# Kernel tuning notes

Measured on AMD Instinct MI355X. Metric: run time of the kernel, lower is better.

## Reference

```python
import jax, jax.numpy as jnp
import numpy as np

B, P, T, F, H, C = 256, 5, 256, 128, 512, 60
R_ON = 0.05    # open ratio of the phased-LSTM time gate
ALPHA = 0.001  # leak during the closed phase


def setup_inputs() -> dict:
    key = jax.random.key(0)
    ks = jax.random.split(key, 8)
    D = P * F  # flattened per-step input to the cell
    s = 1.0 / np.sqrt(H)
    inputs = jax.random.normal(ks[0], (B, P, T, F), dtype=jnp.float32)
    Wx = jax.random.uniform(ks[1], (D, 4 * H), minval=-s, maxval=s, dtype=jnp.float32)
    Wh = jax.random.uniform(ks[2], (H, 4 * H), minval=-s, maxval=s, dtype=jnp.float32)
    b = jax.random.uniform(ks[3], (4 * H,), minval=-s, maxval=s, dtype=jnp.float32)
    # time-gate params: periods spread log-uniformly up to seq length, random phase
    tau = jnp.exp(jax.random.uniform(ks[4], (H,), minval=0.0, maxval=np.log(T), dtype=jnp.float32)) + 1.0
    shift = jax.random.uniform(ks[5], (H,), minval=0.0, maxval=float(T), dtype=jnp.float32)
    fc_w = jax.random.uniform(ks[6], (H, C), minval=-s, maxval=s, dtype=jnp.float32)
    fc_b = jax.random.uniform(ks[7], (C,), minval=-s, maxval=s, dtype=jnp.float32)
    return {"inputs": inputs, "Wx": Wx, "Wh": Wh, "b": b,
            "tau": tau, "shift": shift, "fc_w": fc_w, "fc_b": fc_b}


def _time_gate(t, tau, shift):
    # phase in [0,1); triangular opening of width r_on, alpha leak otherwise
    phi = jnp.mod(t - shift, tau) / tau  # (H,)
    up = 2.0 * phi / R_ON
    down = 2.0 - up
    return jnp.where(phi < 0.5 * R_ON, up,
                     jnp.where(phi < R_ON, down, ALPHA * phi))


def reference(inputs, Wx, Wh, b, tau, shift, fc_w, fc_b):
    # inputs: (B, P, T, F) -> time-major flattened (T, B, P*F)
    x_seq = jnp.transpose(inputs, (2, 0, 1, 3)).reshape(T, B, P * F)
    times = jnp.arange(T, dtype=jnp.float32)

    h0 = jnp.zeros((B, H), dtype=inputs.dtype)
    c0 = jnp.zeros((B, H), dtype=inputs.dtype)

    def step(carry, xt):
        h, c = carry
        x, t = xt
        gates = x @ Wx + h @ Wh + b          # (B, 4H)
        i, f, g, o = jnp.split(gates, 4, axis=-1)
        i = jax.nn.sigmoid(i)
        f = jax.nn.sigmoid(f)
        g = jnp.tanh(g)
        o = jax.nn.sigmoid(o)
        c_tilde = f * c + i * g              # LSTM cell proposal
        h_tilde = o * jnp.tanh(c_tilde)
        k = _time_gate(t, tau, shift)        # (H,) phased time gate
        c_new = k * c_tilde + (1.0 - k) * c
        h_new = k * h_tilde + (1.0 - k) * h
        return (h_new, c_new), None

    (hT, _), _ = jax.lax.scan(step, (h0, c0), (x_seq, times))
    logits = hT @ fc_w + fc_b                # (B, C)
    return jax.nn.log_softmax(logits, axis=-1)
```

## Files before the change

### kernel.cpp

```cpp
#include <hip/hip_runtime.h>
#include <math.h>

#define T_STEPS 256
#define BATCH   256
#define HID     512
#define DIN     640
#define NCOL    2048
#define NCLASS  60
#define KSTEPS  36
#define KX      20
#define KH      16

typedef float f32x4 __attribute__((ext_vector_type(4)));
typedef short s16x8 __attribute__((ext_vector_type(8)));

#define WF_OFF   4096
#define HB0_OFF  4722688
#define HB1_OFF  4984832
#define HPL_OFF  5246976
#define XF_OFF   5771264
#define WS_NEED  89657344ULL

__device__ __forceinline__ unsigned short f2bf(float x) {
    union { float f; unsigned u; } v; v.f = x;
    unsigned r = v.u + 0x7fffu + ((v.u >> 16) & 1u);
    return (unsigned short)(r >> 16);
}

__device__ __forceinline__ s16x8 pack8(float4 a, float4 b) {
    s16x8 r;
    r[0] = (short)f2bf(a.x); r[1] = (short)f2bf(a.y);
    r[2] = (short)f2bf(a.z); r[3] = (short)f2bf(a.w);
    r[4] = (short)f2bf(b.x); r[5] = (short)f2bf(b.y);
    r[6] = (short)f2bf(b.z); r[7] = (short)f2bf(b.w);
    return r;
}

__device__ __forceinline__ float fsigmoid(float x) {
    return __builtin_amdgcn_rcpf(1.f + __expf(-x));
}
__device__ __forceinline__ float ftanh_f(float x) {
    float e = __expf(-2.f * fabsf(x));
    float r = (1.f - e) * __builtin_amdgcn_rcpf(1.f + e);
    return copysignf(r, x);
}

__global__ __launch_bounds__(256) void pack_w_kernel(
    const float* __restrict__ Wx, const float* __restrict__ Wh,
    unsigned short* __restrict__ Wf)
{
    int g = blockIdx.x * 256 + threadIdx.x;
    int nb  = g / (KSTEPS * 64);
    int rem = g - nb * (KSTEPS * 64);
    int ks = rem >> 6;
    int lane = rem & 63;
    int gate = nb & 3, hg = nb >> 2;
    int n = gate * 512 + hg * 16 + (lane & 15);
    int kbase = ks * 32 + (lane >> 4) * 8;
    s16x8 frag;
    #pragma unroll
    for (int j = 0; j < 8; j++) {
        int k = kbase + j;
        float v = (k < DIN) ? Wx[(size_t)k * NCOL + n]
                            : Wh[(size_t)(k - DIN) * NCOL + n];
        frag[j] = (short)f2bf(v);
    }
    *(s16x8*)(Wf + (size_t)g * 8) = frag;
}

__global__ __launch_bounds__(256) void xf_kernel(
    const float* __restrict__ x, unsigned short* __restrict__ xf)
{
    int bid = blockIdx.x;
    int t = bid >> 4, mbg = bid & 15;
    for (int it = threadIdx.x; it < 1280; it += 256) {
        int ks = it >> 6, lane = it & 63;
        int row = mbg * 16 + (lane & 15);
        int k = ks * 32 + (lane >> 4) * 8;
        int p = k >> 7, f = k & 127;
        const float* sp = x + ((size_t)(row * 5 + p) * 256 + t) * 128 + f;
        float4 u0 = *(const float4*)sp;
        float4 u1 = *(const float4*)(sp + 4);
        s16x8 o = pack8(u0, u1);
        *(s16x8*)(xf + ((size_t)bid * 1280 + it) * 8) = o;
    }
}

__global__ __launch_bounds__(256, 1) void plstm_persist3(
    const unsigned short* __restrict__ xf,
    const unsigned short* __restrict__ Wf,
    unsigned short* __restrict__ hb0,
    unsigned short* __restrict__ hb1,
    float* __restrict__ hplain,
    const float* __restrict__ bias,
    const float* __restrict__ tau,
    const float* __restrict__ shift,
    int* __restrict__ ctl)
{
    __shared__ unsigned short wfl[4 * KSTEPS * 64 * 8];
    __shared__ float gl[32][65];
    __shared__ int protflag;

    int tid = threadIdx.x;
    int lane = tid & 63, w = tid >> 6;
    int bid = blockIdx.x;
    int mt = bid & 7, hg = bid >> 3;
    int quad = lane >> 4, l16 = lane & 15;
    int mb = w & 1;
    int n0 = (w >> 1) * 2;

    int xcc = __builtin_amdgcn_s_getreg((31 << 11) | (0 << 6) | 20);
    if (tid == 0) {
        __hip_atomic_store(&ctl[544 + bid], xcc + 1, __ATOMIC_RELAXED,
                           __HIP_MEMORY_SCOPE_AGENT);
        asm volatile("s_waitcnt vmcnt(0)" ::: "memory");
        __hip_atomic_fetch_add(&ctl[512], 1, __ATOMIC_RELAXED,
                               __HIP_MEMORY_SCOPE_AGENT);
        while (__hip_atomic_load(&ctl[512], __ATOMIC_RELAXED,
                                 __HIP_MEMORY_SCOPE_AGENT) < 256)
            __builtin_amdgcn_s_sleep(1);
    }

    {
        const s16x8* src = (const s16x8*)(Wf + (size_t)(hg * 4) * KSTEPS * 64 * 8);
        s16x8* dst = (s16x8*)wfl;
        #pragma unroll
        for (int i = 0; i < 36; i++)
            dst[i * 256 + tid] = src[i * 256 + tid];
    }
    __syncthreads();

    if (w == 0) {
        int pred = 1;
        if (lane < 32) {
            int v = __hip_atomic_load(&ctl[544 + mt + 8 * lane], __ATOMIC_RELAXED,
                                      __HIP_MEMORY_SCOPE_AGENT);
            pred = (v == xcc + 1);
        }
        unsigned long long bal = __ballot(pred);
        if (lane == 0) protflag = (bal == ~0ull) ? 1 : 0;
    }
    __syncthreads();
    int fast = protflag;

    int b_l = tid >> 3;
    int j0  = (tid & 7) * 2;
    int bG  = mt * 32 + b_l;
    int jG0 = hg * 16 + j0;
    float bi[2], bff[2], bg[2], bo[2], phs[2], itau[2];
    #pragma unroll
    for (int r = 0; r < 2; r++) {
        int jG = jG0 + r;
        bi[r] = bias[jG];        bff[r] = bias[512 + jG];
        bg[r] = bias[1024 + jG]; bo[r] = bias[1536 + jG];
        float tj = tau[jG], sj = shift[jG];
        itau[r] = 1.f / tj;
        float ph = fmodf(-sj, tj);
        ph = (ph < 0.f) ? ph + tj : ph;
        phs[r] = ph * itau[r];
    }
    float creg[2] = {0.f, 0.f}, hreg[2] = {0.f, 0.f};
    size_t pub32;
    {
        int mb2 = bG >> 4, khs2 = jG0 >> 5;
        int ln  = (bG & 15) + ((jG0 >> 3) & 3) * 16;
        pub32 = ((((size_t)mb2 * KH + khs2) * 64 + ln) * 8 + (jG0 & 7)) >> 1;
    }

    int mbg = mt * 2 + mb;
    volatile int* fcv = (volatile int*)&ctl[256 + mt * 32];
    unsigned long long fca = (unsigned long long)(ctl + 256 + mt * 32);
    int* scnt = &ctl[mt * 32];

    s16x8 xa[KX];
    {
        const s16x8* x0 = (const s16x8*)xf + (size_t)mbg * KX * 64;
        #pragma unroll
        for (int ks = 0; ks < KX; ks++) xa[ks] = x0[ks * 64 + lane];
    }

    for (int t = 0; t < T_STEPS; t++) {
        f32x4 acc0 = {0.f, 0.f, 0.f, 0.f}, acc1 = acc0;
        #pragma unroll
        for (int ks = 0; ks < KX; ks++) {
            s16x8 b0 = *(const s16x8*)(wfl + (((n0    ) * KSTEPS + ks) * 64 + lane) * 8);
            s16x8 b1 = *(const s16x8*)(wfl + (((n0 + 1) * KSTEPS + ks) * 64 + lane) * 8);
            acc0 = __builtin_amdgcn_mfma_f32_16x16x32_bf16(xa[ks], b0, acc0, 0, 0, 0);
            acc1 = __builtin_amdgcn_mfma_f32_16x16x32_bf16(xa[ks], b1, acc1, 0, 0, 0);
        }

        if (tid == 0) {
            if (fast) {
                int v;
                do {
                    asm volatile("buffer_inv" ::: "memory");
                    v = *fcv;
                } while (v < 32 * t);
            } else {
                while (__hip_atomic_load(scnt, __ATOMIC_RELAXED,
                                         __HIP_MEMORY_SCOPE_AGENT) < 32 * t)
                    __builtin_amdgcn_s_sleep(1);
            }
        }
        __syncthreads();

        const unsigned short* hsrc = (t & 1) ? hb1 : hb0;
        unsigned short*       hdst = (t & 1) ? hb0 : hb1;

        if (fast) {
            asm volatile("buffer_inv" ::: "memory");
            const s16x8* hs = (const s16x8*)hsrc + (size_t)mbg * KH * 64;
            #pragma unroll
            for (int khs = 0; khs < KH; khs++) {
                s16x8 a  = hs[khs * 64 + lane];
                int ks = KX + khs;
                s16x8 b0 = *(const s16x8*)(wfl + (((n0    ) * KSTEPS + ks) * 64 + lane) * 8);
                s16x8 b1 = *(const s16x8*)(wfl + (((n0 + 1) * KSTEPS + ks) * 64 + lane) * 8);
                acc0 = __builtin_amdgcn_mfma_f32_16x16x32_bf16(a, b0, acc0, 0, 0, 0);
                acc1 = __builtin_amdgcn_mfma_f32_16x16x32_bf16(a, b1, acc1, 0, 0, 0);
            }
        } else {
            const unsigned long long* hq =
                (const unsigned long long*)(hsrc + ((size_t)mbg * KH * 64) * 8);
            #pragma unroll
            for (int khs = 0; khs < KH; khs++) {
                union { unsigned long long q[2]; s16x8 v; } a;
                size_t base = ((size_t)khs * 64 + lane) * 2;
                a.q[0] = __hip_atomic_load(hq + base,     __ATOMIC_RELAXED,
                                           __HIP_MEMORY_SCOPE_AGENT);
                a.q[1] = __hip_atomic_load(hq + base + 1, __ATOMIC_RELAXED,
                                           __HIP_MEMORY_SCOPE_AGENT);
                int ks = KX + khs;
                s16x8 b0 = *(const s16x8*)(wfl + (((n0    ) * KSTEPS + ks) * 64 + lane) * 8);
                s16x8 b1 = *(const s16x8*)(wfl + (((n0 + 1) * KSTEPS + ks) * 64 + lane) * 8);
                acc0 = __builtin_amdgcn_mfma_f32_16x16x32_bf16(a.v, b0, acc0, 0, 0, 0);
                acc1 = __builtin_amdgcn_mfma_f32_16x16x32_bf16(a.v, b1, acc1, 0, 0, 0);
            }
        }

        int colb = n0 * 16 + l16;
        int rowb = mb * 16 + quad * 4;
        #pragma unroll
        for (int r = 0; r < 4; r++) {
            gl[rowb + r][colb]      = acc0[r];
            gl[rowb + r][colb + 16] = acc1[r];
        }
        __syncthreads();

        {
            int tp = (t < T_STEPS - 1) ? t + 1 : t;
            const s16x8* xn = (const s16x8*)xf + ((size_t)tp * 16 + mbg) * KX * 64;
            #pragma unroll
            for (int ks = 0; ks < KX; ks++) xa[ks] = xn[ks * 64 + lane];
        }

        float hn2[2];
        #pragma unroll
        for (int r = 0; r < 2; r++) {
            int j_l = j0 + r;
            float iv = fsigmoid(gl[b_l][j_l]      + bi[r]);
            float fv = fsigmoid(gl[b_l][16 + j_l] + bff[r]);
            float gv = ftanh_f (gl[b_l][32 + j_l] + bg[r]);
            float ov = fsigmoid(gl[b_l][48 + j_l] + bo[r]);
            float ct = fv * creg[r] + iv * gv;
            float ht = ov * ftanh_f(ct);
            float ph = phs[r];
            float kg = (ph < 0.025f) ? 40.f * ph
                     : ((ph < 0.05f) ? 2.f - 40.f * ph : 0.001f * ph);
            creg[r] = kg * ct + (1.f - kg) * creg[r];
            hreg[r] = kg * ht + (1.f - kg) * hreg[r];
            hn2[r] = hreg[r];
            ph += itau[r];
            phs[r] = (ph >= 1.f) ? ph - 1.f : ph;
        }
        unsigned pv = (unsigned)f2bf(hn2[0]) | ((unsigned)f2bf(hn2[1]) << 16);
        if (fast) {
            ((unsigned*)hdst)[pub32] = pv;
        } else {
            __hip_atomic_store((unsigned*)hdst + pub32, pv, __ATOMIC_RELAXED,
                               __HIP_MEMORY_SCOPE_AGENT);
        }
        if (t == T_STEPS - 1) {
            hplain[(size_t)bG * HID + jG0]     = hn2[0];
            hplain[(size_t)bG * HID + jG0 + 1] = hn2[1];
        }
        __syncthreads();

        if (tid == 0) {
            if (fast) {
                int one = 1;
                asm volatile("global_atomic_add %0, %1, off"
                             :: "v"(fca), "v"(one) : "memory");
            } else {
                __hip_atomic_fetch_add(scnt, 1, __ATOMIC_RELAXED,
                                       __HIP_MEMORY_SCOPE_AGENT);
            }
        }
    }
}

__global__ __launch_bounds__(256, 1) void plstm_persist(
    const float* __restrict__ x,
    const unsigned short* __restrict__ Wf,
    unsigned short* __restrict__ hb0,
    unsigned short* __restrict__ hb1,
    float* __restrict__ hplain,
    const float* __restrict__ bias,
    const float* __restrict__ tau,
    const float* __restrict__ shift,
    int* __restrict__ cnt)
{
    __shared__ unsigned short wfl[4 * KSTEPS * 64 * 8];
    __shared__ float gl[32][65];

    int tid = threadIdx.x;
    int lane = tid & 63, w = tid >> 6;
    int mt = blockIdx.x & 7, hg = blockIdx.x >> 3;
    int quad = lane >> 4, l16 = lane & 15;
    int mb = w & 1;
    int n0 = (w >> 1) * 2;

    {
        const s16x8* src = (const s16x8*)(Wf + (size_t)(hg * 4) * KSTEPS * 64 * 8);
        s16x8* dst = (s16x8*)wfl;
        #pragma unroll
        for (int i = 0; i < 36; i++)
            dst[i * 256 + tid] = src[i * 256 + tid];
    }

    int b_l  = tid >> 3;
    int j_l0 = (tid & 7) * 2;
    int bG   = mt * 32 + b_l;
    int jG0  = hg * 16 + j_l0;
    float bi[2], bff[2], bg[2], bo[2], tj[2], sj[2];
    #pragma unroll
    for (int r = 0; r < 2; r++) {
        int jG = jG0 + r;
        bi[r] = bias[jG];        bff[r] = bias[512 + jG];
        bg[r] = bias[1024 + jG]; bo[r] = bias[1536 + jG];
        tj[r] = tau[jG];         sj[r] = shift[jG];
    }
    float creg[2] = {0.f, 0.f}, hreg[2] = {0.f, 0.f};
    size_t pub32;
    {
        int mb2  = bG >> 4, khs2 = jG0 >> 5;
        int ln   = (bG & 15) + ((jG0 >> 3) & 3) * 16;
        pub32 = ((((size_t)mb2 * KH + khs2) * 64 + ln) * 8 + (jG0 & 7)) >> 1;
    }
    __syncthreads();

    int rowA = mt * 32 + mb * 16 + l16;
    int mbg  = mt * 2 + mb;
    int* mycnt = cnt + mt * 32;

    for (int t = 0; t < T_STEPS; t++) {
        f32x4 acc0 = {0.f,0.f,0.f,0.f}, acc1 = acc0;
        #pragma unroll
        for (int ks = 0; ks < KX; ks++) {
            int k = ks * 32 + quad * 8;
            int p = k >> 7, f = k & 127;
            const float* sp = x + ((size_t)(rowA * 5 + p) * 256 + t) * 128 + f;
            float4 u0 = *(const float4*)sp;
            float4 u1 = *(const float4*)(sp + 4);
            s16x8 a = pack8(u0, u1);
            s16x8 b0 = *(const s16x8*)(wfl + (((n0    ) * KSTEPS + ks) * 64 + lane) * 8);
            s16x8 b1 = *(const s16x8*)(wfl + (((n0 + 1) * KSTEPS + ks) * 64 + lane) * 8);
            acc0 = __builtin_amdgcn_mfma_f32_16x16x32_bf16(a, b0, acc0, 0, 0, 0);
            acc1 = __builtin_amdgcn_mfma_f32_16x16x32_bf16(a, b1, acc1, 0, 0, 0);
        }

        if (tid == 0) {
            while (__hip_atomic_load(mycnt, __ATOMIC_RELAXED,
                                     __HIP_MEMORY_SCOPE_AGENT) < 32 * t)
                __builtin_amdgcn_s_sleep(1);
        }
        __syncthreads();

        const unsigned short* hsrc = (t & 1) ? hb1 : hb0;
        unsigned short*       hdst = (t & 1) ? hb0 : hb1;

        const unsigned long long* hq =
            (const unsigned long long*)(hsrc + ((size_t)mbg * KH * 64) * 8);
        #pragma unroll
        for (int khs = 0; khs < KH; khs++) {
            union { unsigned long long q[2]; s16x8 v; } a;
            size_t base = ((size_t)khs * 64 + lane) * 2;
            a.q[0] = __hip_atomic_load(hq + base,     __ATOMIC_RELAXED,
                                       __HIP_MEMORY_SCOPE_AGENT);
            a.q[1] = __hip_atomic_load(hq + base + 1, __ATOMIC_RELAXED,
                                       __HIP_MEMORY_SCOPE_AGENT);
            int ks = KX + khs;
            s16x8 b0 = *(const s16x8*)(wfl + (((n0    ) * KSTEPS + ks) * 64 + lane) * 8);
            s16x8 b1 = *(const s16x8*)(wfl + (((n0 + 1) * KSTEPS + ks) * 64 + lane) * 8);
            acc0 = __builtin_amdgcn_mfma_f32_16x16x32_bf16(a.v, b0, acc0, 0, 0, 0);
            acc1 = __builtin_amdgcn_mfma_f32_16x16x32_bf16(a.v, b1, acc1, 0, 0, 0);
        }

        int colb = n0 * 16 + l16;
        int rowb = mb * 16 + quad * 4;
        #pragma unroll
        for (int r = 0; r < 4; r++) {
            gl[rowb + r][colb]      = acc0[r];
            gl[rowb + r][colb + 16] = acc1[r];
        }
        __syncthreads();

        float hn2[2];
        #pragma unroll
        for (int r = 0; r < 2; r++) {
            int j_l = j_l0 + r;
            float iv = gl[b_l][j_l]      + bi[r];
            float fv = gl[b_l][16 + j_l] + bff[r];
            float gv = gl[b_l][32 + j_l] + bg[r];
            float ov = gl[b_l][48 + j_l] + bo[r];
            iv = 1.f / (1.f + expf(-iv));
            fv = 1.f / (1.f + expf(-fv));
            gv = tanhf(gv);
            ov = 1.f / (1.f + expf(-ov));
            float ct = fv * creg[r] + iv * gv;
            float ht = ov * tanhf(ct);
            float phi = fmodf((float)t - sj[r], tj[r]);
            phi = (phi < 0.f) ? phi + tj[r] : phi;
            phi /= tj[r];
            float kg = (phi < 0.025f) ? 40.f * phi
                     : ((phi < 0.05f) ? 2.f - 40.f * phi : 0.001f * phi);
            creg[r] = kg * ct + (1.f - kg) * creg[r];
            hreg[r] = kg * ht + (1.f - kg) * hreg[r];
            hn2[r] = hreg[r];
        }
        unsigned pv = (unsigned)f2bf(hn2[0]) | ((unsigned)f2bf(hn2[1]) << 16);
        __hip_atomic_store((unsigned*)hdst + pub32, pv, __ATOMIC_RELAXED,
                           __HIP_MEMORY_SCOPE_AGENT);
        if (t == T_STEPS - 1) {
            hplain[(size_t)bG * HID + jG0]     = hn2[0];
            hplain[(size_t)bG * HID + jG0 + 1] = hn2[1];
        }
        __syncthreads();

        if (tid == 0)
            __hip_atomic_fetch_add(mycnt, 1, __ATOMIC_RELAXED,
                                   __HIP_MEMORY_SCOPE_AGENT);
    }
}

__global__ __launch_bounds__(64) void fc_kernel(
    const float* __restrict__ hplain, const float* __restrict__ fcw,
    const float* __restrict__ fcb, float* __restrict__ out)
{
    int b = blockIdx.x, lane = threadIdx.x;
    float logit = -INFINITY;
    if (lane < NCLASS) {
        float s = fcb[lane];
        const float* hp = hplain + (size_t)b * HID;
        #pragma unroll 8
        for (int k = 0; k < HID; k++)
            s += hp[k] * fcw[(size_t)k * NCLASS + lane];
        logit = s;
    }
    float m = logit;
    for (int off = 32; off > 0; off >>= 1)
        m = fmaxf(m, __shfl_xor(m, off, 64));
    float e = (lane < NCLASS) ? expf(logit - m) : 0.f;
    float se = e;
    for (int off = 32; off > 0; off >>= 1)
        se += __shfl_xor(se, off, 64);
    if (lane < NCLASS)
        out[(size_t)b * NCLASS + lane] = logit - m - logf(se);
}

extern "C" void kernel_launch(void* const* d_in, const int* in_sizes, int n_in,
                              void* d_out, int out_size, void* d_ws, size_t ws_size,
                              hipStream_t stream)
{
    const float* x     = (const float*)d_in[0];
    const float* Wx    = (const float*)d_in[1];
    const float* Wh    = (const float*)d_in[2];
    const float* bias  = (const float*)d_in[3];
    const float* tau   = (const float*)d_in[4];
    const float* shift = (const float*)d_in[5];
    const float* fcw   = (const float*)d_in[6];
    const float* fcb   = (const float*)d_in[7];
    float* out = (float*)d_out;
    char* ws = (char*)d_ws;

    int*            ctl    = (int*)ws;
    unsigned short* Wf     = (unsigned short*)(ws + WF_OFF);
    unsigned short* hb0    = (unsigned short*)(ws + HB0_OFF);
    unsigned short* hb1    = (unsigned short*)(ws + HB1_OFF);
    float*          hplain = (float*)(ws + HPL_OFF);
    unsigned short* xfb    = (unsigned short*)(ws + XF_OFF);

    hipMemsetAsync(ws, 0, 4096, stream);
    hipMemsetAsync(ws + HB0_OFF, 0, 262144, stream);

    pack_w_kernel<<<dim3(1152), dim3(256), 0, stream>>>(Wx, Wh, Wf);

    if (ws_size >= WS_NEED) {
        xf_kernel<<<dim3(4096), dim3(256), 0, stream>>>(x, xfb);
        plstm_persist3<<<dim3(256), dim3(256), 0, stream>>>(
            xfb, Wf, hb0, hb1, hplain, bias, tau, shift, ctl);
    } else {
        plstm_persist<<<dim3(256), dim3(256), 0, stream>>>(
            x, Wf, hb0, hb1, hplain, bias, tau, shift, ctl);
    }

    fc_kernel<<<dim3(256), dim3(64), 0, stream>>>(hplain, fcw, fcb, out);
}
```

Baseline: 1.025 ms.

## Replace atomic step counter with per-block flag array and overlap x prefetch

The fast-path inter-block barrier changes from one atomic counter to a per-block flag array. Each block writes its step number into its own slot, and wave 0 polls all 32 flags in parallel with a ballot. The h operand loads are hoisted into registers ahead of the MFMA loop, and the next step's x prefetch moves before the end-of-step barrier, which now waits only on the earlier stores using a partial vmcnt. The aim is to cut barrier latency on the sequential critical path. The hand-tuned waitcnt and the plain flag stores make memory ordering fragile.

```diff
diff --git a/kernel.cpp b/kernel.cpp
--- a/kernel.cpp
+++ b/kernel.cpp
@@ -168,8 +168,7 @@
     }
 
     int mbg = mt * 2 + mb;
-    volatile int* fcv = (volatile int*)&ctl[256 + mt * 32];
-    unsigned long long fca = (unsigned long long)(ctl + 256 + mt * 32);
+    int* flg  = &ctl[256 + mt * 32];
     int* scnt = &ctl[mt * 32];
 
     s16x8 xa[KX];
@@ -189,14 +188,17 @@
             acc1 = __builtin_amdgcn_mfma_f32_16x16x32_bf16(xa[ks], b1, acc1, 0, 0, 0);
         }
 
-        if (tid == 0) {
-            if (fast) {
-                int v;
-                do {
+        if (fast) {
+            if (w == 0) {
+                for (;;) {
                     asm volatile("buffer_inv" ::: "memory");
-                    v = *fcv;
-                } while (v < 32 * t);
-            } else {
+                    int v = t;
+                    if (lane < 32) v = *(volatile int*)(flg + lane);
+                    if (__ballot(v >= t) == ~0ull) break;
+                }
+            }
+        } else {
+            if (tid == 0) {
                 while (__hip_atomic_load(scnt, __ATOMIC_RELAXED,
                                          __HIP_MEMORY_SCOPE_AGENT) < 32 * t)
                     __builtin_amdgcn_s_sleep(1);
@@ -210,14 +212,17 @@
         if (fast) {
             asm volatile("buffer_inv" ::: "memory");
             const s16x8* hs = (const s16x8*)hsrc + (size_t)mbg * KH * 64;
+            s16x8 ha[KH];
+            #pragma unroll
+            for (int khs = 0; khs < KH; khs++)
+                ha[khs] = hs[khs * 64 + lane];
             #pragma unroll
             for (int khs = 0; khs < KH; khs++) {
-                s16x8 a  = hs[khs * 64 + lane];
                 int ks = KX + khs;
                 s16x8 b0 = *(const s16x8*)(wfl + (((n0    ) * KSTEPS + ks) * 64 + lane) * 8);
                 s16x8 b1 = *(const s16x8*)(wfl + (((n0 + 1) * KSTEPS + ks) * 64 + lane) * 8);
-                acc0 = __builtin_amdgcn_mfma_f32_16x16x32_bf16(a, b0, acc0, 0, 0, 0);
-                acc1 = __builtin_amdgcn_mfma_f32_16x16x32_bf16(a, b1, acc1, 0, 0, 0);
+                acc0 = __builtin_amdgcn_mfma_f32_16x16x32_bf16(ha[khs], b0, acc0, 0, 0, 0);
+                acc1 = __builtin_amdgcn_mfma_f32_16x16x32_bf16(ha[khs], b1, acc1, 0, 0, 0);
             }
         } else {
             const unsigned long long* hq =
@@ -247,13 +252,6 @@
         }
         __syncthreads();
 
-        {
-            int tp = (t < T_STEPS - 1) ? t + 1 : t;
-            const s16x8* xn = (const s16x8*)xf + ((size_t)tp * 16 + mbg) * KX * 64;
-            #pragma unroll
-            for (int ks = 0; ks < KX; ks++) xa[ks] = xn[ks * 64 + lane];
-        }
-
         float hn2[2];
         #pragma unroll
         for (int r = 0; r < 2; r++) {
@@ -273,6 +271,7 @@
             ph += itau[r];
             phs[r] = (ph >= 1.f) ? ph - 1.f : ph;
         }
+
         unsigned pv = (unsigned)f2bf(hn2[0]) | ((unsigned)f2bf(hn2[1]) << 16);
         if (fast) {
             ((unsigned*)hdst)[pub32] = pv;
@@ -284,13 +283,25 @@
             hplain[(size_t)bG * HID + jG0]     = hn2[0];
             hplain[(size_t)bG * HID + jG0 + 1] = hn2[1];
         }
-        __syncthreads();
+        asm volatile("" ::: "memory");
+
+        {
+            int tp = (t < T_STEPS - 1) ? t + 1 : t;
+            const s16x8* xn = (const s16x8*)xf + ((size_t)tp * 16 + mbg) * KX * 64;
+            #pragma unroll
+            for (int ks = 0; ks < KX; ks++) xa[ks] = xn[ks * 64 + lane];
+        }
+
+        if (fast) {
+            asm volatile("s_waitcnt vmcnt(20)" ::: "memory");
+            __builtin_amdgcn_s_barrier();
+        } else {
+            __syncthreads();
+        }
 
         if (tid == 0) {
             if (fast) {
-                int one = 1;
-                asm volatile("global_atomic_add %0, %1, off"
-                             :: "v"(fca), "v"(one) : "memory");
+                *(volatile int*)(flg + hg) = t + 1;
             } else {
                 __hip_atomic_fetch_add(scnt, 1, __ATOMIC_RELAXED,
                                        __HIP_MEMORY_SCOPE_AGENT);
```

Measured after the change: 1.144 ms. +11.6%, slower.

## Replace atomic counter barrier with per-block flags polled by a wavefront

Applied to the files above, without the earlier changes.

The per-step cross-block barrier in the fast path changes from one shared atomic counter, polled by thread 0, to an array of per-block step flags. Each block writes its own flag with a plain volatile store, and every wavefront polls 32 flags in parallel with a ballot, so the __syncthreads after the wait is gone. The next step's x-fragment loads are double-buffered (xaA/xaB, loop unrolled by two) and issued before the MMAs, so they overlap with compute. There is no longer an explicit buffer_inv before the h reads, and the flag store has no release fence, so memory-ordering correctness relies on the hardware.

```diff
diff --git a/kernel.cpp b/kernel.cpp
--- a/kernel.cpp
+++ b/kernel.cpp
@@ -86,6 +86,124 @@
     }
 }
 
+#define PLSTM_STEP(T, CUR, NXT)                                               \
+  {                                                                           \
+         \
+    int tp_ = ((T) < T_STEPS - 1) ? (T) + 1 : (T);                            \
+    const s16x8* xn_ = (const s16x8*)xf + ((size_t)tp_ * 16 + mbg) * KX * 64; \
+    _Pragma("unroll")                                                         \
+    for (int ks = 0; ks < KX; ks++) NXT[ks] = xn_[ks * 64 + lane];            \
+                                                                 \
+    f32x4 acc0 = {0.f, 0.f, 0.f, 0.f}, acc1 = acc0;                           \
+    _Pragma("unroll")                                                         \
+    for (int ks = 0; ks < KX; ks++) {                                         \
+      s16x8 b0 = *(const s16x8*)(wfl + (((n0    ) * KSTEPS + ks) * 64 + lane) * 8); \
+      s16x8 b1 = *(const s16x8*)(wfl + (((n0 + 1) * KSTEPS + ks) * 64 + lane) * 8); \
+      acc0 = __builtin_amdgcn_mfma_f32_16x16x32_bf16(CUR[ks], b0, acc0, 0, 0, 0);   \
+      acc1 = __builtin_amdgcn_mfma_f32_16x16x32_bf16(CUR[ks], b1, acc1, 0, 0, 0);   \
+    }                                                                         \
+                                                      \
+    if (fast) {                                                               \
+      for (;;) {                                                              \
+        asm volatile("buffer_inv" ::: "memory");              \
+        int v_ = (T);                                                         \
+        if (lane < 32) v_ = *(volatile int*)(flg + lane);                     \
+        if (__ballot(v_ >= (T)) == ~0ull) break;                              \
+      }                                                                       \
+    } else {                                                                  \
+      if (tid == 0) {                                                         \
+        while (__hip_atomic_load(scnt, __ATOMIC_RELAXED,                      \
+                                 __HIP_MEMORY_SCOPE_AGENT) < 32 * (T))        \
+          __builtin_amdgcn_s_sleep(1);                                        \
+      }                                                                       \
+      __syncthreads();                                                        \
+    }                                                                         \
+    const unsigned short* hsrc = ((T) & 1) ? hb1 : hb0;                       \
+    unsigned short*       hdst = ((T) & 1) ? hb0 : hb1;                       \
+                                                                 \
+    if (fast) {                                                               \
+      const s16x8* hs_ = (const s16x8*)hsrc + (size_t)mbg * KH * 64;          \
+      _Pragma("unroll")                                                       \
+      for (int khs = 0; khs < KH; khs++) {                                    \
+        s16x8 a_ = hs_[khs * 64 + lane];                                      \
+        int ks = KX + khs;                                                    \
+        s16x8 b0 = *(const s16x8*)(wfl + (((n0    ) * KSTEPS + ks) * 64 + lane) * 8); \
+        s16x8 b1 = *(const s16x8*)(wfl + (((n0 + 1) * KSTEPS + ks) * 64 + lane) * 8); \
+        acc0 = __builtin_amdgcn_mfma_f32_16x16x32_bf16(a_, b0, acc0, 0, 0, 0);\
+        acc1 = __builtin_amdgcn_mfma_f32_16x16x32_bf16(a_, b1, acc1, 0, 0, 0);\
+      }                                                                       \
+    } else {                                                                  \
+      const unsigned long long* hq_ =                                         \
+          (const unsigned long long*)(hsrc + ((size_t)mbg * KH * 64) * 8);    \
+      _Pragma("unroll")                                                       \
+      for (int khs = 0; khs < KH; khs++) {                                    \
+        union { unsigned long long q[2]; s16x8 v; } a_;                       \
+        size_t base_ = ((size_t)khs * 64 + lane) * 2;                         \
+        a_.q[0] = __hip_atomic_load(hq_ + base_,     __ATOMIC_RELAXED,        \
+                                    __HIP_MEMORY_SCOPE_AGENT);                \
+        a_.q[1] = __hip_atomic_load(hq_ + base_ + 1, __ATOMIC_RELAXED,        \
+                                    __HIP_MEMORY_SCOPE_AGENT);                \
+        int ks = KX + khs;                                                    \
+        s16x8 b0 = *(const s16x8*)(wfl + (((n0    ) * KSTEPS + ks) * 64 + lane) * 8); \
+        s16x8 b1 = *(const s16x8*)(wfl + (((n0 + 1) * KSTEPS + ks) * 64 + lane) * 8); \
+        acc0 = __builtin_amdgcn_mfma_f32_16x16x32_bf16(a_.v, b0, acc0, 0, 0, 0);      \
+        acc1 = __builtin_amdgcn_mfma_f32_16x16x32_bf16(a_.v, b1, acc1, 0, 0, 0);      \
+      }                                                                       \
+    }                                                                         \
+                     \
+    {                                                                         \
+      int colb_ = n0 * 16 + l16;                                              \
+      int rowb_ = mb * 16 + quad * 4;                                         \
+      _Pragma("unroll")                                                       \
+      for (int r = 0; r < 4; r++) {                                           \
+        gl[rowb_ + r][colb_]      = acc0[r];                                  \
+        gl[rowb_ + r][colb_ + 16] = acc1[r];                                  \
+      }                                                                       \
+    }                                                                         \
+    __syncthreads();                                                          \
+                                                                \
+    float hn2_[2];                                                            \
+    _Pragma("unroll")                                                         \
+    for (int r = 0; r < 2; r++) {                                             \
+      int j_l = j0 + r;                                                       \
+      float iv = fsigmoid(gl[b_l][j_l]      + bi[r]);                         \
+      float fv = fsigmoid(gl[b_l][16 + j_l] + bff[r]);                        \
+      float gv = ftanh_f (gl[b_l][32 + j_l] + bg[r]);                         \
+      float ov = fsigmoid(gl[b_l][48 + j_l] + bo[r]);                         \
+      float ct = fv * creg[r] + iv * gv;                                      \
+      float ht = ov * ftanh_f(ct);                                            \
+      float ph = phs[r];                                                      \
+      float kg = (ph < 0.025f) ? 40.f * ph                                    \
+               : ((ph < 0.05f) ? 2.f - 40.f * ph : 0.001f * ph);              \
+      creg[r] = kg * ct + (1.f - kg) * creg[r];                               \
+      hreg[r] = kg * ht + (1.f - kg) * hreg[r];                               \
+      hn2_[r] = hreg[r];                                                      \
+      ph += itau[r];                                                          \
+      phs[r] = (ph >= 1.f) ? ph - 1.f : ph;                                   \
+    }                                                                         \
+    unsigned pv_ = (unsigned)f2bf(hn2_[0]) | ((unsigned)f2bf(hn2_[1]) << 16); \
+    if (fast) {                                                               \
+      ((unsigned*)hdst)[pub32] = pv_;                \
+    } else {                                                                  \
+      __hip_atomic_store((unsigned*)hdst + pub32, pv_, __ATOMIC_RELAXED,      \
+                         __HIP_MEMORY_SCOPE_AGENT);                           \
+    }                                                                         \
+    if ((T) == T_STEPS - 1) {                                                 \
+      hplain[(size_t)bG * HID + jG0]     = hn2_[0];                           \
+      hplain[(size_t)bG * HID + jG0 + 1] = hn2_[1];                           \
+    }                                                                         \
+    __syncthreads();      \
+                                                    \
+    if (tid == 0) {                                                           \
+      if (fast) {                                                             \
+        *(volatile int*)(flg + hg) = (T) + 1;     \
+      } else {                                                                \
+        __hip_atomic_fetch_add(scnt, 1, __ATOMIC_RELAXED,                     \
+                               __HIP_MEMORY_SCOPE_AGENT);                     \
+      }                                                                       \
+    }                                                                         \
+  }
+
 __global__ __launch_bounds__(256, 1) void plstm_persist3(
     const unsigned short* __restrict__ xf,
     const unsigned short* __restrict__ Wf,
@@ -168,134 +286,19 @@
     }
 
     int mbg = mt * 2 + mb;
-    volatile int* fcv = (volatile int*)&ctl[256 + mt * 32];
-    unsigned long long fca = (unsigned long long)(ctl + 256 + mt * 32);
+    int* flg  = &ctl[256 + mt * 32];
     int* scnt = &ctl[mt * 32];
 
-    s16x8 xa[KX];
+    s16x8 xaA[KX], xaB[KX];
     {
         const s16x8* x0 = (const s16x8*)xf + (size_t)mbg * KX * 64;
         #pragma unroll
-        for (int ks = 0; ks < KX; ks++) xa[ks] = x0[ks * 64 + lane];
-    }
-
-    for (int t = 0; t < T_STEPS; t++) {
-        f32x4 acc0 = {0.f, 0.f, 0.f, 0.f}, acc1 = acc0;
-        #pragma unroll
-        for (int ks = 0; ks < KX; ks++) {
-            s16x8 b0 = *(const s16x8*)(wfl + (((n0    ) * KSTEPS + ks) * 64 + lane) * 8);
-            s16x8 b1 = *(const s16x8*)(wfl + (((n0 + 1) * KSTEPS + ks) * 64 + lane) * 8);
-            acc0 = __builtin_amdgcn_mfma_f32_16x16x32_bf16(xa[ks], b0, acc0, 0, 0, 0);
-            acc1 = __builtin_amdgcn_mfma_f32_16x16x32_bf16(xa[ks], b1, acc1, 0, 0, 0);
-        }
-
-        if (tid == 0) {
-            if (fast) {
-                int v;
-                do {
-                    asm volatile("buffer_inv" ::: "memory");
-                    v = *fcv;
-                } while (v < 32 * t);
-            } else {
-                while (__hip_atomic_load(scnt, __ATOMIC_RELAXED,
-                                         __HIP_MEMORY_SCOPE_AGENT) < 32 * t)
-                    __builtin_amdgcn_s_sleep(1);
-            }
-        }
-        __syncthreads();
-
-        const unsigned short* hsrc = (t & 1) ? hb1 : hb0;
-        unsigned short*       hdst = (t & 1) ? hb0 : hb1;
-
-        if (fast) {
-            asm volatile("buffer_inv" ::: "memory");
-            const s16x8* hs = (const s16x8*)hsrc + (size_t)mbg * KH * 64;
-            #pragma unroll
-            for (int khs = 0; khs < KH; khs++) {
-                s16x8 a  = hs[khs * 64 + lane];
-                int ks = KX + khs;
-                s16x8 b0 = *(const s16x8*)(wfl + (((n0    ) * KSTEPS + ks) * 64 + lane) * 8);
-                s16x8 b1 = *(const s16x8*)(wfl + (((n0 + 1) * KSTEPS + ks) * 64 + lane) * 8);
-                acc0 = __builtin_amdgcn_mfma_f32_16x16x32_bf16(a, b0, acc0, 0, 0, 0);
-                acc1 = __builtin_amdgcn_mfma_f32_16x16x32_bf16(a, b1, acc1, 0, 0, 0);
-            }
-        } else {
-            const unsigned long long* hq =
-                (const unsigned long long*)(hsrc + ((size_t)mbg * KH * 64) * 8);
-            #pragma unroll
-            for (int khs = 0; khs < KH; khs++) {
-                union { unsigned long long q[2]; s16x8 v; } a;
-                size_t base = ((size_t)khs * 64 + lane) * 2;
-                a.q[0] = __hip_atomic_load(hq + base,     __ATOMIC_RELAXED,
-                                           __HIP_MEMORY_SCOPE_AGENT);
-                a.q[1] = __hip_atomic_load(hq + base + 1, __ATOMIC_RELAXED,
-                                           __HIP_MEMORY_SCOPE_AGENT);
-                int ks = KX + khs;
-                s16x8 b0 = *(const s16x8*)(wfl + (((n0    ) * KSTEPS + ks) * 64 + lane) * 8);
-                s16x8 b1 = *(const s16x8*)(wfl + (((n0 + 1) * KSTEPS + ks) * 64 + lane) * 8);
-                acc0 = __builtin_amdgcn_mfma_f32_16x16x32_bf16(a.v, b0, acc0, 0, 0, 0);
-                acc1 = __builtin_amdgcn_mfma_f32_16x16x32_bf16(a.v, b1, acc1, 0, 0, 0);
-            }
-        }
-
-        int colb = n0 * 16 + l16;
-        int rowb = mb * 16 + quad * 4;
-        #pragma unroll
-        for (int r = 0; r < 4; r++) {
-            gl[rowb + r][colb]      = acc0[r];
-            gl[rowb + r][colb + 16] = acc1[r];
-        }
-        __syncthreads();
-
-        {
-            int tp = (t < T_STEPS - 1) ? t + 1 : t;
-            const s16x8* xn = (const s16x8*)xf + ((size_t)tp * 16 + mbg) * KX * 64;
-            #pragma unroll
-            for (int ks = 0; ks < KX; ks++) xa[ks] = xn[ks * 64 + lane];
-        }
-
-        float hn2[2];
-        #pragma unroll
-        for (int r = 0; r < 2; r++) {
-            int j_l = j0 + r;
-            float iv = fsigmoid(gl[b_l][j_l]      + bi[r]);
-            float fv = fsigmoid(gl[b_l][16 + j_l] + bff[r]);
-            float gv = ftanh_f (gl[b_l][32 + j_l] + bg[r]);
-            float ov = fsigmoid(gl[b_l][48 + j_l] + bo[r]);
-            float ct = fv * creg[r] + iv * gv;
-            float ht = ov * ftanh_f(ct);
-            float ph = phs[r];
-            float kg = (ph < 0.025f) ? 40.f * ph
-                     : ((ph < 0.05f) ? 2.f - 40.f * ph : 0.001f * ph);
-            creg[r] = kg * ct + (1.f - kg) * creg[r];
-            hreg[r] = kg * ht + (1.f - kg) * hreg[r];
-            hn2[r] = hreg[r];
-            ph += itau[r];
-            phs[r] = (ph >= 1.f) ? ph - 1.f : ph;
-        }
-        unsigned pv = (unsigned)f2bf(hn2[0]) | ((unsigned)f2bf(hn2[1]) << 16);
-        if (fast) {
-            ((unsigned*)hdst)[pub32] = pv;
-        } else {
-            __hip_atomic_store((unsigned*)hdst + pub32, pv, __ATOMIC_RELAXED,
-                               __HIP_MEMORY_SCOPE_AGENT);
-        }
-        if (t == T_STEPS - 1) {
-            hplain[(size_t)bG * HID + jG0]     = hn2[0];
-            hplain[(size_t)bG * HID + jG0 + 1] = hn2[1];
-        }
-        __syncthreads();
-
-        if (tid == 0) {
-            if (fast) {
-                int one = 1;
-                asm volatile("global_atomic_add %0, %1, off"
-                             :: "v"(fca), "v"(one) : "memory");
-            } else {
-                __hip_atomic_fetch_add(scnt, 1, __ATOMIC_RELAXED,
-                                       __HIP_MEMORY_SCOPE_AGENT);
-            }
-        }
+        for (int ks = 0; ks < KX; ks++) xaA[ks] = x0[ks * 64 + lane];
+    }
+
+    for (int tt = 0; tt < T_STEPS; tt += 2) {
+        PLSTM_STEP(tt,     xaA, xaB)
+        PLSTM_STEP(tt + 1, xaB, xaA)
     }
 }
 
```

After: 1.255 ms. 1.22x slower.
